# Kernel tuning notes

Hardware: AMD Instinct MI355X
Metric: run time of the kernel (lower is better)

Reference implementation:

```python
import jax, jax.numpy as jnp
import numpy as np

NUM_HEADS = 16
ROPE_BASE = 10000.0
NEG_INF = float('-inf')


def _rotate_half_interleaved(x):
    # x: [..., d]; interleaved rotation: (-x2, x1) pairs
    x1 = x[..., ::2]
    x2 = x[..., 1::2]
    return jnp.stack((-x2, x1), axis=-1).reshape(x.shape)


def _rope_tables(seq_len, head_dim, dtype):
    inv_freq = 1.0 / (ROPE_BASE ** (jnp.arange(0, head_dim, 2, dtype=jnp.float32) / head_dim))
    pos = jnp.arange(seq_len, dtype=jnp.float32)
    freqs = pos[:, None] * inv_freq[None, :]          # [S, d/2]
    emb = jnp.concatenate((freqs, freqs), axis=-1)    # [S, d]  (HF-style concat, as in source)
    return jnp.cos(emb).astype(dtype), jnp.sin(emb).astype(dtype)


def setup_inputs() -> dict:
    key = jax.random.key(0)
    ks = jax.random.split(key, 4)
    B, S, H = 2, 2048, 2048
    scale = 0.02
    x = jax.random.normal(ks[0], (B, S, H), dtype=jnp.float32)
    qkv_w = jax.random.normal(ks[1], (3 * H, H), dtype=jnp.float32) * scale
    qkv_b = jnp.zeros((3 * H,), dtype=jnp.float32)
    out_w = jax.random.normal(ks[2], (H, H), dtype=jnp.float32) * scale
    out_b = jnp.zeros((H,), dtype=jnp.float32)
    attention_mask = jnp.ones((B, S), dtype=jnp.int32)
    return {"x": x, "attention_mask": attention_mask, "qkv_w": qkv_w,
            "qkv_b": qkv_b, "out_w": out_w, "out_b": out_b}


def reference(x, attention_mask, qkv_w, qkv_b, out_w, out_b):
    B, S, H = x.shape
    nh = NUM_HEADS
    hd = H // nh
    scale = hd ** -0.5

    qkv = x @ qkv_w.T + qkv_b                            # [B,S,3H]
    qkv = qkv.reshape(B, S, 3, nh, hd).transpose(2, 0, 3, 1, 4)  # [3,B,nh,S,hd]
    q, k, v = qkv[0], qkv[1], qkv[2]

    cos, sin = _rope_tables(S, hd, x.dtype)              # [S,hd]
    cos = cos[None, None, :, :]
    sin = sin[None, None, :, :]
    q = q * cos + _rotate_half_interleaved(q) * sin
    k = k * cos + _rotate_half_interleaved(k) * sin

    scores = jnp.einsum('bhqd,bhkd->bhqk', q, k) * scale  # [B,nh,S,S]
    causal = jnp.triu(jnp.ones((S, S), dtype=bool), k=1)
    scores = jnp.where(causal[None, None], NEG_INF, scores)
    key_mask = (attention_mask == 0)[:, None, None, :]    # [B,1,1,S]
    scores = jnp.where(key_mask, NEG_INF, scores)

    weights = jax.nn.softmax(scores, axis=-1)
    attn = jnp.einsum('bhqk,bhkd->bhqd', weights, v)       # [B,nh,S,hd]
    attn = attn.transpose(0, 2, 1, 3).reshape(B, S, H)
    return attn @ out_w.T + out_b
```

## Files before the change

### kernel.cpp

```cpp
#include <hip/hip_runtime.h>

typedef __bf16 bf16;
typedef __bf16 bf16x2 __attribute__((ext_vector_type(2)));
typedef __bf16 bf16x4 __attribute__((ext_vector_type(4)));
typedef __bf16 bf16x8 __attribute__((ext_vector_type(8)));
typedef float f32x4 __attribute__((ext_vector_type(4)));
typedef float f32x16 __attribute__((ext_vector_type(16)));

#define MFMA_BF16(a, b, c) __builtin_amdgcn_mfma_f32_16x16x32_bf16(a, b, c, 0, 0, 0)
#define MFMA32(a, b, c)    __builtin_amdgcn_mfma_f32_32x32x16_bf16(a, b, c, 0, 0, 0)

__device__ __forceinline__ void async16(const void* g, void* l) {
    __builtin_amdgcn_global_load_lds(
        (const __attribute__((address_space(1))) void*)g,
        (__attribute__((address_space(3))) void*)l,
        16, 0, 0);
}

__device__ __forceinline__ unsigned pack2(float a, float b) {
    bf16x2 t; t[0] = (bf16)a; t[1] = (bf16)b;
    return __builtin_bit_cast(unsigned, t);
}

__device__ __forceinline__ void cvt8_body(const float* __restrict__ in,
                                          bf16* __restrict__ out, int blk) {
    int i = (blk * 256 + (int)threadIdx.x) * 8;
    float4 a = *(const float4*)(in + i);
    float4 b = *(const float4*)(in + i + 4);
    bf16x8 o;
    o[0] = (bf16)a.x; o[1] = (bf16)a.y; o[2] = (bf16)a.z; o[3] = (bf16)a.w;
    o[4] = (bf16)b.x; o[5] = (bf16)b.y; o[6] = (bf16)b.z; o[7] = (bf16)b.w;
    *(bf16x8*)(out + i) = o;
}

__global__ void prep(const float* __restrict__ x, const float* __restrict__ qkvw,
                     const float* __restrict__ outw, const int* __restrict__ am,
                     bf16* __restrict__ xb, bf16* __restrict__ wqkv, bf16* __restrict__ wout,
                     float* __restrict__ cosT, float* __restrict__ sinT,
                     float* __restrict__ mbias) {
    int blk = blockIdx.x;
    if (blk < 4096)        cvt8_body(x,    xb,   blk);
    else if (blk < 10240)  cvt8_body(qkvw, wqkv, blk - 4096);
    else if (blk < 12288)  cvt8_body(outw, wout, blk - 10240);
    else {
        int i = (blk - 12288) * 256 + threadIdx.x;
        int s = i >> 6, fi = i & 63;
        float inv = exp2f(-(float)fi * (13.287712379549449f / 64.0f));
        float ang = (float)s * inv;
        cosT[i] = cosf(ang);
        sinT[i] = sinf(ang);
        if (i < 2 * 2048) mbias[i] = (am[i] == 0) ? -1.4427e30f : 0.0f;
    }
}

template <int EPI>
__global__ void __launch_bounds__(256, 2)
gemm_bt(const bf16* __restrict__ A, const bf16* __restrict__ Bt,
        const float* __restrict__ bias, float* __restrict__ Cf,
        bf16* __restrict__ qb, bf16* __restrict__ kb, bf16* __restrict__ vtb,
        const float* __restrict__ cosT, const float* __restrict__ sinT,
        int M, int N, int K) {
    __shared__ __align__(16) bf16 sA[128 * 64];
    __shared__ __align__(16) bf16 sB[128 * 64];
    const int tid  = threadIdx.x;
    const int lane = tid & 63;
    const int quad = lane >> 4, l15 = lane & 15;
    const int wid = tid >> 6, wm = wid >> 1, wn = wid & 1;
    const int bm = blockIdx.x, bn = blockIdx.y;

    f32x4 acc[4][4];
#pragma unroll
    for (int i = 0; i < 4; i++)
#pragma unroll
        for (int j = 0; j < 4; j++)
#pragma unroll
            for (int c = 0; c < 4; c++) acc[i][j][c] = 0.0f;

    const int r0 = tid >> 3, x0 = tid & 7;
    const int g0 = x0 ^ (r0 & 7);
    const bf16* pa = A  + (size_t)(bm * 128 + r0) * K + g0 * 8;
    const bf16* pb = Bt + (size_t)(bn * 128 + r0) * K + g0 * 8;
    bf16* la = sA + tid * 8;
    bf16* lb = sB + tid * 8;
    const size_t gstep = (size_t)32 * K;

    for (int k0 = 0; k0 < K; k0 += 64) {
#pragma unroll
        for (int i = 0; i < 4; i++) {
            async16(pa + i * gstep, la + i * 2048);
            async16(pb + i * gstep, lb + i * 2048);
        }
        pa += 64; pb += 64;
        __syncthreads();
#pragma unroll
        for (int ks = 0; ks < 2; ks++) {
            bf16x8 af[4], bfr[4];
#pragma unroll
            for (int i = 0; i < 4; i++) {
                int r = wm * 64 + i * 16 + l15;
                int x = (ks * 4 + quad) ^ (r & 7);
                af[i] = *(const bf16x8*)(sA + r * 64 + x * 8);
            }
#pragma unroll
            for (int i = 0; i < 4; i++) {
                int r = wn * 64 + i * 16 + l15;
                int x = (ks * 4 + quad) ^ (r & 7);
                bfr[i] = *(const bf16x8*)(sB + r * 64 + x * 8);
            }
#pragma unroll
            for (int mi = 0; mi < 4; mi++)
#pragma unroll
                for (int ni = 0; ni < 4; ni++)
                    acc[mi][ni] = MFMA_BF16(af[mi], bfr[ni], acc[mi][ni]);
        }
        __syncthreads();
    }

    if (EPI == 0) {
#pragma unroll
        for (int mi = 0; mi < 4; mi++)
#pragma unroll
            for (int ni = 0; ni < 4; ni++) {
                int row0 = bm * 128 + wm * 64 + mi * 16 + quad * 4;
                int col  = bn * 128 + wn * 64 + ni * 16 + l15;
                float bv = bias[col];
#pragma unroll
                for (int r = 0; r < 4; r++)
                    Cf[(size_t)(row0 + r) * N + col] = acc[mi][ni][r] + bv;
            }
    } else {
#pragma unroll
        for (int mi = 0; mi < 4; mi++)
#pragma unroll
            for (int ni = 0; ni < 4; ni++) {
                int col   = bn * 128 + wn * 64 + ni * 16 + l15;
                int which = col >> 11;
                int hcol  = col & 2047;
                int h = hcol >> 7, d = hcol & 127;
                float bv = bias[col];
#pragma unroll
                for (int r = 0; r < 4; r++) {
                    int row = bm * 128 + wm * 64 + mi * 16 + quad * 4 + r;
                    int b = row >> 11, s = row & 2047;
                    float v  = acc[mi][ni][r] + bv;
                    float vp = __shfl_xor(v, 1, 64);
                    float ov = v;
                    if (which < 2) {
                        float c  = cosT[(s << 6) + (d & 63)];
                        float sn = sinT[(s << 6) + (d & 63)];
                        ov = v * c + ((d & 1) ? vp : -vp) * sn;
                    }
                    if (which == 0) ov *= 0.12751743f;
                    size_t bh = (size_t)(b * 16 + h);
                    if (which == 0)      qb[(bh * 2048 + s) * 128 + d] = (bf16)ov;
                    else if (which == 1) kb[(bh * 2048 + s) * 128 + d] = (bf16)ov;
                    else                 vtb[(bh * 128 + d) * 2048 + s] = (bf16)ov;
                }
            }
    }
}

__global__ void __launch_bounds__(256, 2)
fattn(const bf16* __restrict__ Q, const bf16* __restrict__ Kg,
      const bf16* __restrict__ Vt, const float* __restrict__ mbias,
      bf16* __restrict__ O, float* __restrict__ Opart, float* __restrict__ mlpart) {
    __shared__ __align__(16) bf16 sK[2][64 * 128];
    __shared__ __align__(16) bf16 sV[2][128 * 64];
    const int tid = threadIdx.x, lane = tid & 63, w = tid >> 6;
    const int l31 = lane & 31, half = lane >> 5;
    const int id = (int)blockIdx.x;
    const int bh = id & 31, v = id >> 5;
    const int p = v >> 1, role = v & 1;
    const int qa = 15 - p;
    const int n1 = role ? (15 - 2 * p) : 17;

    const bf16* Qb  = Q  + (size_t)bh * 2048 * 128;
    const bf16* Kbh = Kg + (size_t)bh * 2048 * 128;
    const bf16* Vbh = Vt + (size_t)bh * 128 * 2048;
    const int b = bh >> 4, hh = bh & 15;
    const float* mbb = mbias + b * 2048;

    const int swk = (l31 & 15) ^ (l31 >> 4);
    const int swv = (l31 & 7) ^ ((l31 >> 3) & 3);
    const int rk = tid >> 4, xk = tid & 15, gkb = xk ^ rk;
    const int rv = tid >> 3, xv = tid & 7;
    const int gv = xv ^ (rv & 7) ^ ((rv >> 3) & 3);

    auto KT = [&](int t) { return role ? (t < n1 ? 17 + t : t - n1) : t; };

    int qt = qa;
    int myq  = qt * 128 + w * 32 + l31;
    int qmin = qt * 128 + w * 32;

    bf16x8 qf[8];
#pragma unroll
    for (int kq = 0; kq < 8; kq++)
        qf[kq] = *(const bf16x8*)(Qb + (size_t)myq * 128 + kq * 16 + half * 8);

    f32x16 oacc[4];
#pragma unroll
    for (int dt = 0; dt < 4; dt++)
#pragma unroll
        for (int c = 0; c < 16; c++) oacc[dt][c] = 0.0f;
    float m_s = -3e38f, l_s = 0.0f;

    {
        int kb0 = KT(0) * 64;
#pragma unroll
        for (int i = 0; i < 4; i++) {
            async16(Kbh + (size_t)(kb0 + rk + i * 16) * 128 + (gkb ^ (i & 1)) * 8,
                    &sK[0][(i * 256 + tid) * 8]);
            async16(Vbh + (size_t)(rv + i * 32) * 2048 + kb0 + gv * 8,
                    &sV[0][(i * 256 + tid) * 8]);
        }
    }
    __syncthreads();

    for (int t = 0; t < 17; t++) {
        if (role && t == n1) {
            float lf = l_s + __shfl_xor(l_s, 32, 64);
            size_t slot = (size_t)(bh * 8 + (qa - 8)) * 2 + 1;
            float* op = Opart + slot * 16384 + (size_t)(w * 32 + l31) * 128;
#pragma unroll
            for (int dt = 0; dt < 4; dt++)
#pragma unroll
                for (int g = 0; g < 4; g++) {
                    float4 o4 = make_float4(oacc[dt][g * 4 + 0], oacc[dt][g * 4 + 1],
                                            oacc[dt][g * 4 + 2], oacc[dt][g * 4 + 3]);
                    *(float4*)(op + dt * 32 + 8 * g + 4 * half) = o4;
                }
            if (half == 0) {
                float* mp = mlpart + (slot * 128 + (w * 32 + l31)) * 2;
                mp[0] = m_s; mp[1] = lf;
            }
#pragma unroll
            for (int dt = 0; dt < 4; dt++)
#pragma unroll
                for (int c = 0; c < 16; c++) oacc[dt][c] = 0.0f;
            m_s = -3e38f; l_s = 0.0f;
            qt = p;
            myq  = qt * 128 + w * 32 + l31;
            qmin = qt * 128 + w * 32;
#pragma unroll
            for (int kq = 0; kq < 8; kq++)
                qf[kq] = *(const bf16x8*)(Qb + (size_t)myq * 128 + kq * 16 + half * 8);
        }

        const int kb0 = KT(t) * 64;
        const int buf = t & 1;
        if (t + 1 < 17) {
            const int nb0 = KT(t + 1) * 64;
#pragma unroll
            for (int i = 0; i < 4; i++) {
                async16(Kbh + (size_t)(nb0 + rk + i * 16) * 128 + (gkb ^ (i & 1)) * 8,
                        &sK[buf ^ 1][(i * 256 + tid) * 8]);
                async16(Vbh + (size_t)(rv + i * 32) * 2048 + nb0 + gv * 8,
                        &sV[buf ^ 1][(i * 256 + tid) * 8]);
            }
        }
        const bf16* sKb = sK[buf];
        const bf16* sVb = sV[buf];

        f32x16 sacc[2];
#pragma unroll
        for (int tt = 0; tt < 2; tt++)
#pragma unroll
            for (int c = 0; c < 16; c++) sacc[tt][c] = 0.0f;
#pragma unroll
        for (int kq = 0; kq < 8; kq++) {
#pragma unroll
            for (int tt = 0; tt < 2; tt++) {
                int row = tt * 32 + l31;
                int x = (kq * 2 + half) ^ swk;
                bf16x8 kf = *(const bf16x8*)(sKb + row * 128 + x * 8);
                sacc[tt] = MFMA32(kf, qf[kq], sacc[tt]);
            }
        }

        float pmx[4];
#pragma unroll
        for (int r2 = 0; r2 < 4; r2++) pmx[r2] = -3e38f;
        if (kb0 + 63 < qmin) {
#pragma unroll
            for (int tt = 0; tt < 2; tt++)
#pragma unroll
                for (int g = 0; g < 4; g++) {
                    float4 mb4 = *(const float4*)(mbb + kb0 + tt * 32 + 8 * g + 4 * half);
#pragma unroll
                    for (int r2 = 0; r2 < 4; r2++) {
                        float vv = sacc[tt][g * 4 + r2] + ((const float*)&mb4)[r2];
                        sacc[tt][g * 4 + r2] = vv;
                        pmx[r2] = fmaxf(pmx[r2], vv);
                    }
                }
        } else {
#pragma unroll
            for (int tt = 0; tt < 2; tt++)
#pragma unroll
                for (int g = 0; g < 4; g++) {
                    float4 mb4 = *(const float4*)(mbb + kb0 + tt * 32 + 8 * g + 4 * half);
#pragma unroll
                    for (int r2 = 0; r2 < 4; r2++) {
                        int sk = kb0 + tt * 32 + 8 * g + 4 * half + r2;
                        float vv = sacc[tt][g * 4 + r2] + ((const float*)&mb4)[r2];
                        vv = (sk > myq) ? -1e30f : vv;
                        sacc[tt][g * 4 + r2] = vv;
                        pmx[r2] = fmaxf(pmx[r2], vv);
                    }
                }
        }
        float mx = fmaxf(fmaxf(pmx[0], pmx[1]), fmaxf(pmx[2], pmx[3]));

        mx = fmaxf(mx, __shfl_xor(mx, 32, 64));
        float mnew  = fmaxf(m_s, mx);
        float alpha = exp2f(m_s - mnew);
        float prs[4];
#pragma unroll
        for (int r2 = 0; r2 < 4; r2++) prs[r2] = 0.0f;
#pragma unroll
        for (int tt = 0; tt < 2; tt++)
#pragma unroll
            for (int c = 0; c < 16; c++) {
                float pe = exp2f(sacc[tt][c] - mnew);
                sacc[tt][c] = pe;
                prs[c & 3] += pe;
            }
        float rs = (prs[0] + prs[1]) + (prs[2] + prs[3]);
        l_s = l_s * alpha + rs;
        m_s = mnew;
#pragma unroll
        for (int dt = 0; dt < 4; dt++) oacc[dt] *= alpha;

#pragma unroll
        for (int tt = 0; tt < 2; tt++) {
            unsigned w8[8];
#pragma unroll
            for (int i = 0; i < 8; i++)
                w8[i] = pack2(sacc[tt][2 * i], sacc[tt][2 * i + 1]);
#pragma unroll
            for (int s2 = 0; s2 < 2; s2++) {
                const int bse = 4 * s2;
                unsigned a0 = half ? w8[bse]     : w8[bse + 2];
                unsigned a1 = half ? w8[bse + 1] : w8[bse + 3];
                unsigned z0 = (unsigned)__shfl_xor((int)a0, 32, 64);
                unsigned z1 = (unsigned)__shfl_xor((int)a1, 32, 64);
                union { unsigned u[4]; bf16x8 vv; } pu;
                pu.u[0] = half ? z0 : w8[bse];
                pu.u[1] = half ? z1 : w8[bse + 1];
                pu.u[2] = half ? w8[bse + 2] : z0;
                pu.u[3] = half ? w8[bse + 3] : z1;
                bf16x8 pf = pu.vv;
                const int c = (tt * 2 + s2) * 2 + half;
#pragma unroll
                for (int dt = 0; dt < 4; dt++) {
                    int row = dt * 32 + l31;
                    int x = c ^ swv;
                    bf16x8 vf = *(const bf16x8*)(sVb + row * 64 + x * 8);
                    oacc[dt] = MFMA32(vf, pf, oacc[dt]);
                }
            }
        }
        __syncthreads();
    }

    float lf = l_s + __shfl_xor(l_s, 32, 64);
    if (role == 0) {
        size_t slot = (size_t)(bh * 8 + (qa - 8)) * 2 + 0;
        float* op = Opart + slot * 16384 + (size_t)(w * 32 + l31) * 128;
#pragma unroll
        for (int dt = 0; dt < 4; dt++)
#pragma unroll
            for (int g = 0; g < 4; g++) {
                float4 o4 = make_float4(oacc[dt][g * 4 + 0], oacc[dt][g * 4 + 1],
                                        oacc[dt][g * 4 + 2], oacc[dt][g * 4 + 3]);
                *(float4*)(op + dt * 32 + 8 * g + 4 * half) = o4;
            }
        if (half == 0) {
            float* mp = mlpart + (slot * 128 + (w * 32 + l31)) * 2;
            mp[0] = m_s; mp[1] = lf;
        }
    } else {
        float inv = 1.0f / lf;
        size_t base = ((size_t)(b * 2048 + myq)) * 2048 + hh * 128;
#pragma unroll
        for (int dt = 0; dt < 4; dt++)
#pragma unroll
            for (int g = 0; g < 4; g++) {
                bf16x4 o4;
#pragma unroll
                for (int r2 = 0; r2 < 4; r2++) o4[r2] = (bf16)(oacc[dt][g * 4 + r2] * inv);
                *(bf16x4*)(O + base + dt * 32 + 8 * g + 4 * half) = o4;
            }
    }
}

__global__ void combine(const float* __restrict__ Opart, const float* __restrict__ mlpart,
                        bf16* __restrict__ attn) {
    int i = blockIdx.x * 256 + threadIdx.x;
    int dq = (i & 31) * 4;
    int row = i >> 5;
    int qloc = row & 127, ba = row >> 7;
    int ai = ba & 7, bh = ba >> 3;
    const float* mlA = mlpart + ((size_t)(ba * 2 + 0) * 128 + qloc) * 2;
    const float* mlB = mlpart + ((size_t)(ba * 2 + 1) * 128 + qloc) * 2;
    float mA = mlA[0], lA = mlA[1], mB = mlB[0], lB = mlB[1];
    float m = fmaxf(mA, mB);
    float wA = exp2f(mA - m), wB = exp2f(mB - m);
    float inv = 1.0f / (wA * lA + wB * lB);
    float4 oA = *(const float4*)(Opart + (size_t)(ba * 2 + 0) * 16384 + qloc * 128 + dq);
    float4 oB = *(const float4*)(Opart + (size_t)(ba * 2 + 1) * 16384 + qloc * 128 + dq);
    int q = (8 + ai) * 128 + qloc;
    int b = bh >> 4, hh = bh & 15;
    bf16x4 o4;
    o4[0] = (bf16)((wA * oA.x + wB * oB.x) * inv);
    o4[1] = (bf16)((wA * oA.y + wB * oB.y) * inv);
    o4[2] = (bf16)((wA * oA.z + wB * oB.z) * inv);
    o4[3] = (bf16)((wA * oA.w + wB * oB.w) * inv);
    *(bf16x4*)(attn + ((size_t)(b * 2048 + q)) * 2048 + hh * 128 + dq) = o4;
}

extern "C" void kernel_launch(void* const* d_in, const int* in_sizes, int n_in,
                              void* d_out, int out_size, void* d_ws, size_t ws_size,
                              hipStream_t stream) {
    const float* x     = (const float*)d_in[0];
    const int*   am    = (const int*)d_in[1];
    const float* qkvw  = (const float*)d_in[2];
    const float* qkvb  = (const float*)d_in[3];
    const float* outw  = (const float*)d_in[4];
    const float* outb  = (const float*)d_in[5];
    float* out = (float*)d_out;

    char* ws = (char*)d_ws;
    bf16*  xb    = (bf16*)(ws);
    bf16*  wqkv  = (bf16*)(ws + (16ull << 20));
    bf16*  wout  = (bf16*)(ws + (40ull << 20));
    bf16*  qb    = (bf16*)(ws + (48ull << 20));
    bf16*  kb    = (bf16*)(ws + (64ull << 20));
    bf16*  vtb   = (bf16*)(ws + (80ull << 20));
    bf16*  attn  = (bf16*)(ws + (96ull << 20));
    float* cosT  = (float*)(ws + (112ull << 20));
    float* sinT  = (float*)(ws + (113ull << 20));
    float* mbias = (float*)(ws + (114ull << 20));
    float* Opart  = (float*)(ws);
    float* mlpart = (float*)(ws + (32ull << 20));

    prep<<<12800, 256, 0, stream>>>(x, qkvw, outw, am, xb, wqkv, wout, cosT, sinT, mbias);

    gemm_bt<1><<<dim3(32, 48), 256, 0, stream>>>(
        xb, wqkv, qkvb, nullptr, qb, kb, vtb, cosT, sinT, 4096, 6144, 2048);

    fattn<<<dim3(512), 256, 0, stream>>>(qb, kb, vtb, mbias, attn, Opart, mlpart);

    combine<<<4096, 256, 0, stream>>>(Opart, mlpart, attn);

    gemm_bt<0><<<dim3(32, 16), 256, 0, stream>>>(
        attn, wout, outb, out, nullptr, nullptr, nullptr, nullptr, nullptr,
        4096, 2048, 2048);
}
```

Measured before the change: 378.8 us.

## Pair mirrored causal query tiles in one 512-thread block sharing K/V loads

Replaces the split-KV scheme (two 256-thread blocks per query-tile pair, partial outputs, and a separate combine kernel) with one 512-thread block. Its two wave groups each own one of a mirrored pair of query tiles (p and 15-p) and share every streamed K/V tile in LDS. The group with the shorter causal range skips compute on tiles past its diagonal but still takes part in loads and barriers. This removes the combine launch and the fp32 partial-output traffic, and cuts K/V reloads. In exchange the grid drops to 256 blocks, and idle waves wait at barriers during the tail of the longer tile.

```diff
diff --git a/kernel.cpp b/kernel.cpp
--- a/kernel.cpp
+++ b/kernel.cpp
@@ -160,19 +160,19 @@
     }
 }
 
-__global__ void __launch_bounds__(256, 2)
+__global__ void __launch_bounds__(512, 2)
 fattn(const bf16* __restrict__ Q, const bf16* __restrict__ Kg,
       const bf16* __restrict__ Vt, const float* __restrict__ mbias,
-      bf16* __restrict__ O, float* __restrict__ Opart, float* __restrict__ mlpart) {
+      bf16* __restrict__ O) {
     __shared__ __align__(16) bf16 sK[2][64 * 128];
     __shared__ __align__(16) bf16 sV[2][128 * 64];
-    const int tid = threadIdx.x, lane = tid & 63, w = tid >> 6;
+    const int tid = threadIdx.x, lane = tid & 63, wid = tid >> 6;
     const int l31 = lane & 31, half = lane >> 5;
+    const int wq = wid & 3, grp = wid >> 2;
     const int id = (int)blockIdx.x;
-    const int bh = id & 31, v = id >> 5;
-    const int p = v >> 1, role = v & 1;
-    const int qa = 15 - p;
-    const int n1 = role ? (15 - 2 * p) : 17;
+    const int bh = id & 31, p = id >> 5;
+    const int qt  = grp ? p : (15 - p);
+    const int NTb = 32 - 2 * p;
 
     const bf16* Qb  = Q  + (size_t)bh * 2048 * 128;
     const bf16* Kbh = Kg + (size_t)bh * 2048 * 128;
@@ -182,15 +182,13 @@
 
     const int swk = (l31 & 15) ^ (l31 >> 4);
     const int swv = (l31 & 7) ^ ((l31 >> 3) & 3);
-    const int rk = tid >> 4, xk = tid & 15, gkb = xk ^ rk;
-    const int rv = tid >> 3, xv = tid & 7;
+    const int tid2 = tid & 255, jj = tid >> 8;
+    const int rk = tid2 >> 4, gkb = (tid2 & 15) ^ rk;
+    const int rv = tid2 >> 3, xv = tid2 & 7;
     const int gv = xv ^ (rv & 7) ^ ((rv >> 3) & 3);
 
-    auto KT = [&](int t) { return role ? (t < n1 ? 17 + t : t - n1) : t; };
-
-    int qt = qa;
-    int myq  = qt * 128 + w * 32 + l31;
-    int qmin = qt * 128 + w * 32;
+    const int myq  = qt * 128 + wq * 32 + l31;
+    const int qmin = qt * 128 + wq * 32;
 
     bf16x8 qf[8];
 #pragma unroll
@@ -204,219 +202,150 @@
         for (int c = 0; c < 16; c++) oacc[dt][c] = 0.0f;
     float m_s = -3e38f, l_s = 0.0f;
 
-    {
-        int kb0 = KT(0) * 64;
-#pragma unroll
-        for (int i = 0; i < 4; i++) {
-            async16(Kbh + (size_t)(kb0 + rk + i * 16) * 128 + (gkb ^ (i & 1)) * 8,
-                    &sK[0][(i * 256 + tid) * 8]);
-            async16(Vbh + (size_t)(rv + i * 32) * 2048 + kb0 + gv * 8,
-                    &sV[0][(i * 256 + tid) * 8]);
-        }
+#pragma unroll
+    for (int i2 = 0; i2 < 2; i2++) {
+        int i = jj * 2 + i2;
+        async16(Kbh + (size_t)(rk + i * 16) * 128 + (gkb ^ (i & 1)) * 8,
+                &sK[0][(i * 256 + tid2) * 8]);
+        async16(Vbh + (size_t)(rv + i * 32) * 2048 + gv * 8,
+                &sV[0][(i * 256 + tid2) * 8]);
     }
     __syncthreads();
 
-    for (int t = 0; t < 17; t++) {
-        if (role && t == n1) {
-            float lf = l_s + __shfl_xor(l_s, 32, 64);
-            size_t slot = (size_t)(bh * 8 + (qa - 8)) * 2 + 1;
-            float* op = Opart + slot * 16384 + (size_t)(w * 32 + l31) * 128;
-#pragma unroll
-            for (int dt = 0; dt < 4; dt++)
-#pragma unroll
-                for (int g = 0; g < 4; g++) {
-                    float4 o4 = make_float4(oacc[dt][g * 4 + 0], oacc[dt][g * 4 + 1],
-                                            oacc[dt][g * 4 + 2], oacc[dt][g * 4 + 3]);
-                    *(float4*)(op + dt * 32 + 8 * g + 4 * half) = o4;
+    for (int t = 0; t < NTb; t++) {
+        const int kb0 = t * 64;
+        const int buf = t & 1;
+        if (t + 1 < NTb) {
+            const int nb0 = (t + 1) * 64;
+#pragma unroll
+            for (int i2 = 0; i2 < 2; i2++) {
+                int i = jj * 2 + i2;
+                async16(Kbh + (size_t)(nb0 + rk + i * 16) * 128 + (gkb ^ (i & 1)) * 8,
+                        &sK[buf ^ 1][(i * 256 + tid2) * 8]);
+                async16(Vbh + (size_t)(rv + i * 32) * 2048 + nb0 + gv * 8,
+                        &sV[buf ^ 1][(i * 256 + tid2) * 8]);
+            }
+        }
+
+        if (kb0 <= qmin + 31) {
+            const bf16* sKb = sK[buf];
+            const bf16* sVb = sV[buf];
+
+            f32x16 sacc[2];
+#pragma unroll
+            for (int tt = 0; tt < 2; tt++)
+#pragma unroll
+                for (int c = 0; c < 16; c++) sacc[tt][c] = 0.0f;
+#pragma unroll
+            for (int kq = 0; kq < 8; kq++) {
+#pragma unroll
+                for (int tt = 0; tt < 2; tt++) {
+                    int row = tt * 32 + l31;
+                    int x = (kq * 2 + half) ^ swk;
+                    bf16x8 kf = *(const bf16x8*)(sKb + row * 128 + x * 8);
+                    sacc[tt] = MFMA32(kf, qf[kq], sacc[tt]);
                 }
-            if (half == 0) {
-                float* mp = mlpart + (slot * 128 + (w * 32 + l31)) * 2;
-                mp[0] = m_s; mp[1] = lf;
-            }
-#pragma unroll
-            for (int dt = 0; dt < 4; dt++)
-#pragma unroll
-                for (int c = 0; c < 16; c++) oacc[dt][c] = 0.0f;
-            m_s = -3e38f; l_s = 0.0f;
-            qt = p;
-            myq  = qt * 128 + w * 32 + l31;
-            qmin = qt * 128 + w * 32;
-#pragma unroll
-            for (int kq = 0; kq < 8; kq++)
-                qf[kq] = *(const bf16x8*)(Qb + (size_t)myq * 128 + kq * 16 + half * 8);
-        }
-
-        const int kb0 = KT(t) * 64;
-        const int buf = t & 1;
-        if (t + 1 < 17) {
-            const int nb0 = KT(t + 1) * 64;
-#pragma unroll
-            for (int i = 0; i < 4; i++) {
-                async16(Kbh + (size_t)(nb0 + rk + i * 16) * 128 + (gkb ^ (i & 1)) * 8,
-                        &sK[buf ^ 1][(i * 256 + tid) * 8]);
-                async16(Vbh + (size_t)(rv + i * 32) * 2048 + nb0 + gv * 8,
-                        &sV[buf ^ 1][(i * 256 + tid) * 8]);
-            }
-        }
-        const bf16* sKb = sK[buf];
-        const bf16* sVb = sV[buf];
-
-        f32x16 sacc[2];
-#pragma unroll
-        for (int tt = 0; tt < 2; tt++)
-#pragma unroll
-            for (int c = 0; c < 16; c++) sacc[tt][c] = 0.0f;
-#pragma unroll
-        for (int kq = 0; kq < 8; kq++) {
+            }
+
+            float pmx[4];
+#pragma unroll
+            for (int r2 = 0; r2 < 4; r2++) pmx[r2] = -3e38f;
+            if (kb0 + 63 < qmin) {
+#pragma unroll
+                for (int tt = 0; tt < 2; tt++)
+#pragma unroll
+                    for (int g = 0; g < 4; g++) {
+                        float4 mb4 = *(const float4*)(mbb + kb0 + tt * 32 + 8 * g + 4 * half);
+#pragma unroll
+                        for (int r2 = 0; r2 < 4; r2++) {
+                            float vv = sacc[tt][g * 4 + r2] + ((const float*)&mb4)[r2];
+                            sacc[tt][g * 4 + r2] = vv;
+                            pmx[r2] = fmaxf(pmx[r2], vv);
+                        }
+                    }
+            } else {
+#pragma unroll
+                for (int tt = 0; tt < 2; tt++)
+#pragma unroll
+                    for (int g = 0; g < 4; g++) {
+                        float4 mb4 = *(const float4*)(mbb + kb0 + tt * 32 + 8 * g + 4 * half);
+#pragma unroll
+                        for (int r2 = 0; r2 < 4; r2++) {
+                            int sk = kb0 + tt * 32 + 8 * g + 4 * half + r2;
+                            float vv = sacc[tt][g * 4 + r2] + ((const float*)&mb4)[r2];
+                            vv = (sk > myq) ? -1e30f : vv;
+                            sacc[tt][g * 4 + r2] = vv;
+                            pmx[r2] = fmaxf(pmx[r2], vv);
+                        }
+                    }
+            }
+            float mx = fmaxf(fmaxf(pmx[0], pmx[1]), fmaxf(pmx[2], pmx[3]));
+
+            mx = fmaxf(mx, __shfl_xor(mx, 32, 64));
+            float mnew  = fmaxf(m_s, mx);
+            float alpha = exp2f(m_s - mnew);
+            float prs[4];
+#pragma unroll
+            for (int r2 = 0; r2 < 4; r2++) prs[r2] = 0.0f;
+#pragma unroll
+            for (int tt = 0; tt < 2; tt++)
+#pragma unroll
+                for (int c = 0; c < 16; c++) {
+                    float pe = exp2f(sacc[tt][c] - mnew);
+                    sacc[tt][c] = pe;
+                    prs[c & 3] += pe;
+                }
+            float rs = (prs[0] + prs[1]) + (prs[2] + prs[3]);
+            l_s = l_s * alpha + rs;
+            m_s = mnew;
+#pragma unroll
+            for (int dt = 0; dt < 4; dt++) oacc[dt] *= alpha;
+
 #pragma unroll
             for (int tt = 0; tt < 2; tt++) {
-                int row = tt * 32 + l31;
-                int x = (kq * 2 + half) ^ swk;
-                bf16x8 kf = *(const bf16x8*)(sKb + row * 128 + x * 8);
-                sacc[tt] = MFMA32(kf, qf[kq], sacc[tt]);
-            }
-        }
-
-        float pmx[4];
-#pragma unroll
-        for (int r2 = 0; r2 < 4; r2++) pmx[r2] = -3e38f;
-        if (kb0 + 63 < qmin) {
-#pragma unroll
-            for (int tt = 0; tt < 2; tt++)
-#pragma unroll
-                for (int g = 0; g < 4; g++) {
-                    float4 mb4 = *(const float4*)(mbb + kb0 + tt * 32 + 8 * g + 4 * half);
-#pragma unroll
-                    for (int r2 = 0; r2 < 4; r2++) {
-                        float vv = sacc[tt][g * 4 + r2] + ((const float*)&mb4)[r2];
-                        sacc[tt][g * 4 + r2] = vv;
-                        pmx[r2] = fmaxf(pmx[r2], vv);
+                unsigned w8[8];
+#pragma unroll
+                for (int i = 0; i < 8; i++)
+                    w8[i] = pack2(sacc[tt][2 * i], sacc[tt][2 * i + 1]);
+#pragma unroll
+                for (int s2 = 0; s2 < 2; s2++) {
+                    const int bse = 4 * s2;
+                    unsigned a0 = half ? w8[bse]     : w8[bse + 2];
+                    unsigned a1 = half ? w8[bse + 1] : w8[bse + 3];
+                    unsigned z0 = (unsigned)__shfl_xor((int)a0, 32, 64);
+                    unsigned z1 = (unsigned)__shfl_xor((int)a1, 32, 64);
+                    union { unsigned u[4]; bf16x8 vv; } pu;
+                    pu.u[0] = half ? z0 : w8[bse];
+                    pu.u[1] = half ? z1 : w8[bse + 1];
+                    pu.u[2] = half ? w8[bse + 2] : z0;
+                    pu.u[3] = half ? w8[bse + 3] : z1;
+                    bf16x8 pf = pu.vv;
+                    const int c = (tt * 2 + s2) * 2 + half;
+#pragma unroll
+                    for (int dt = 0; dt < 4; dt++) {
+                        int row = dt * 32 + l31;
+                        int x = c ^ swv;
+                        bf16x8 vf = *(const bf16x8*)(sVb + row * 64 + x * 8);
+                        oacc[dt] = MFMA32(vf, pf, oacc[dt]);
                     }
                 }
-        } else {
-#pragma unroll
-            for (int tt = 0; tt < 2; tt++)
-#pragma unroll
-                for (int g = 0; g < 4; g++) {
-                    float4 mb4 = *(const float4*)(mbb + kb0 + tt * 32 + 8 * g + 4 * half);
-#pragma unroll
-                    for (int r2 = 0; r2 < 4; r2++) {
-                        int sk = kb0 + tt * 32 + 8 * g + 4 * half + r2;
-                        float vv = sacc[tt][g * 4 + r2] + ((const float*)&mb4)[r2];
-                        vv = (sk > myq) ? -1e30f : vv;
-                        sacc[tt][g * 4 + r2] = vv;
-                        pmx[r2] = fmaxf(pmx[r2], vv);
-                    }
-                }
-        }
-        float mx = fmaxf(fmaxf(pmx[0], pmx[1]), fmaxf(pmx[2], pmx[3]));
-
-        mx = fmaxf(mx, __shfl_xor(mx, 32, 64));
-        float mnew  = fmaxf(m_s, mx);
-        float alpha = exp2f(m_s - mnew);
-        float prs[4];
-#pragma unroll
-        for (int r2 = 0; r2 < 4; r2++) prs[r2] = 0.0f;
-#pragma unroll
-        for (int tt = 0; tt < 2; tt++)
-#pragma unroll
-            for (int c = 0; c < 16; c++) {
-                float pe = exp2f(sacc[tt][c] - mnew);
-                sacc[tt][c] = pe;
-                prs[c & 3] += pe;
-            }
-        float rs = (prs[0] + prs[1]) + (prs[2] + prs[3]);
-        l_s = l_s * alpha + rs;
-        m_s = mnew;
-#pragma unroll
-        for (int dt = 0; dt < 4; dt++) oacc[dt] *= alpha;
-
-#pragma unroll
-        for (int tt = 0; tt < 2; tt++) {
-            unsigned w8[8];
-#pragma unroll
-            for (int i = 0; i < 8; i++)
-                w8[i] = pack2(sacc[tt][2 * i], sacc[tt][2 * i + 1]);
-#pragma unroll
-            for (int s2 = 0; s2 < 2; s2++) {
-                const int bse = 4 * s2;
-                unsigned a0 = half ? w8[bse]     : w8[bse + 2];
-                unsigned a1 = half ? w8[bse + 1] : w8[bse + 3];
-                unsigned z0 = (unsigned)__shfl_xor((int)a0, 32, 64);
-                unsigned z1 = (unsigned)__shfl_xor((int)a1, 32, 64);
-                union { unsigned u[4]; bf16x8 vv; } pu;
-                pu.u[0] = half ? z0 : w8[bse];
-                pu.u[1] = half ? z1 : w8[bse + 1];
-                pu.u[2] = half ? w8[bse + 2] : z0;
-                pu.u[3] = half ? w8[bse + 3] : z1;
-                bf16x8 pf = pu.vv;
-                const int c = (tt * 2 + s2) * 2 + half;
-#pragma unroll
-                for (int dt = 0; dt < 4; dt++) {
-                    int row = dt * 32 + l31;
-                    int x = c ^ swv;
-                    bf16x8 vf = *(const bf16x8*)(sVb + row * 64 + x * 8);
-                    oacc[dt] = MFMA32(vf, pf, oacc[dt]);
-                }
             }
         }
         __syncthreads();
     }
 
     float lf = l_s + __shfl_xor(l_s, 32, 64);
-    if (role == 0) {
-        size_t slot = (size_t)(bh * 8 + (qa - 8)) * 2 + 0;
-        float* op = Opart + slot * 16384 + (size_t)(w * 32 + l31) * 128;
-#pragma unroll
-        for (int dt = 0; dt < 4; dt++)
-#pragma unroll
-            for (int g = 0; g < 4; g++) {
-                float4 o4 = make_float4(oacc[dt][g * 4 + 0], oacc[dt][g * 4 + 1],
-                                        oacc[dt][g * 4 + 2], oacc[dt][g * 4 + 3]);
-                *(float4*)(op + dt * 32 + 8 * g + 4 * half) = o4;
-            }
-        if (half == 0) {
-            float* mp = mlpart + (slot * 128 + (w * 32 + l31)) * 2;
-            mp[0] = m_s; mp[1] = lf;
-        }
-    } else {
-        float inv = 1.0f / lf;
-        size_t base = ((size_t)(b * 2048 + myq)) * 2048 + hh * 128;
-#pragma unroll
-        for (int dt = 0; dt < 4; dt++)
-#pragma unroll
-            for (int g = 0; g < 4; g++) {
-                bf16x4 o4;
-#pragma unroll
-                for (int r2 = 0; r2 < 4; r2++) o4[r2] = (bf16)(oacc[dt][g * 4 + r2] * inv);
-                *(bf16x4*)(O + base + dt * 32 + 8 * g + 4 * half) = o4;
-            }
-    }
-}
-
-__global__ void combine(const float* __restrict__ Opart, const float* __restrict__ mlpart,
-                        bf16* __restrict__ attn) {
-    int i = blockIdx.x * 256 + threadIdx.x;
-    int dq = (i & 31) * 4;
-    int row = i >> 5;
-    int qloc = row & 127, ba = row >> 7;
-    int ai = ba & 7, bh = ba >> 3;
-    const float* mlA = mlpart + ((size_t)(ba * 2 + 0) * 128 + qloc) * 2;
-    const float* mlB = mlpart + ((size_t)(ba * 2 + 1) * 128 + qloc) * 2;
-    float mA = mlA[0], lA = mlA[1], mB = mlB[0], lB = mlB[1];
-    float m = fmaxf(mA, mB);
-    float wA = exp2f(mA - m), wB = exp2f(mB - m);
-    float inv = 1.0f / (wA * lA + wB * lB);
-    float4 oA = *(const float4*)(Opart + (size_t)(ba * 2 + 0) * 16384 + qloc * 128 + dq);
-    float4 oB = *(const float4*)(Opart + (size_t)(ba * 2 + 1) * 16384 + qloc * 128 + dq);
-    int q = (8 + ai) * 128 + qloc;
-    int b = bh >> 4, hh = bh & 15;
-    bf16x4 o4;
-    o4[0] = (bf16)((wA * oA.x + wB * oB.x) * inv);
-    o4[1] = (bf16)((wA * oA.y + wB * oB.y) * inv);
-    o4[2] = (bf16)((wA * oA.z + wB * oB.z) * inv);
-    o4[3] = (bf16)((wA * oA.w + wB * oB.w) * inv);
-    *(bf16x4*)(attn + ((size_t)(b * 2048 + q)) * 2048 + hh * 128 + dq) = o4;
+    float inv = 1.0f / lf;
+    size_t base = ((size_t)(b * 2048 + myq)) * 2048 + hh * 128;
+#pragma unroll
+    for (int dt = 0; dt < 4; dt++)
+#pragma unroll
+        for (int g = 0; g < 4; g++) {
+            bf16x4 o4;
+#pragma unroll
+            for (int r2 = 0; r2 < 4; r2++) o4[r2] = (bf16)(oacc[dt][g * 4 + r2] * inv);
+            *(bf16x4*)(O + base + dt * 32 + 8 * g + 4 * half) = o4;
+        }
 }
 
 extern "C" void kernel_launch(void* const* d_in, const int* in_sizes, int n_in,
@@ -441,17 +370,13 @@
     float* cosT  = (float*)(ws + (112ull << 20));
     float* sinT  = (float*)(ws + (113ull << 20));
     float* mbias = (float*)(ws + (114ull << 20));
-    float* Opart  = (float*)(ws);
-    float* mlpart = (float*)(ws + (32ull << 20));
 
     prep<<<12800, 256, 0, stream>>>(x, qkvw, outw, am, xb, wqkv, wout, cosT, sinT, mbias);
 
     gemm_bt<1><<<dim3(32, 48), 256, 0, stream>>>(
         xb, wqkv, qkvb, nullptr, qb, kb, vtb, cosT, sinT, 4096, 6144, 2048);
 
-    fattn<<<dim3(512), 256, 0, stream>>>(qb, kb, vtb, mbias, attn, Opart, mlpart);
-
-    combine<<<4096, 256, 0, stream>>>(Opart, mlpart, attn);
+    fattn<<<dim3(256), 512, 0, stream>>>(qb, kb, vtb, mbias, attn);
 
     gemm_bt<0><<<dim3(32, 16), 256, 0, stream>>>(
         attn, wout, outb, out, nullptr, nullptr, nullptr, nullptr, nullptr,
```

New measurement: 394.8 us. 4.2% more time.
